# Performance work log

Hardware: AMD Instinct MI355X
Metric: run time of the kernel (lower is better)

## Reference

```python
import jax, jax.numpy as jnp
import numpy as np

HID = 1024
HEADS = 16
HEAD_DIM = HID // HEADS
LN_EPS = 1e-5  # nn.LayerNorm default (module's self.eps is unused by its LayerNorms)


def layer_norm(x, w, b):
    m = jnp.mean(x, axis=-1, keepdims=True)
    v = jnp.mean(jnp.square(x - m), axis=-1, keepdims=True)
    return (x - m) * jax.lax.rsqrt(v + LN_EPS) * w + b


def setup_inputs() -> dict:
    key = jax.random.key(0)
    ks = jax.random.split(key, 12)
    B, Nq, Nk = 2, 1024, 4096
    s = 1.0 / np.sqrt(HID)
    inp = {
        "queries": jax.random.normal(ks[0], (B, Nq, HID), jnp.float32),
        "kv_tokens": jax.random.normal(ks[1], (B, Nk, HID), jnp.float32),
        "query_type_ids": jax.random.randint(ks[2], (Nq,), 0, 3),
        "kv_type_ids": jax.random.randint(ks[3], (Nk,), 0, 3),
        "kv_padding_mask": jax.random.randint(ks[4], (B, Nk), 0, 2).astype(bool).at[:, 0].set(True),
        "Wq": jax.random.normal(ks[5], (HID, HID), jnp.float32) * s,
        "Wk": jax.random.normal(ks[6], (HID, HID), jnp.float32) * s,
        "Wv": jax.random.normal(ks[7], (HID, HID), jnp.float32) * s,
        "Wo": jax.random.normal(ks[8], (HID, HID), jnp.float32) * s,
        "qn_w": jnp.ones((HID,), jnp.float32), "qn_b": jnp.zeros((HID,), jnp.float32),
        "kvn_w": jnp.ones((HID,), jnp.float32), "kvn_b": jnp.zeros((HID,), jnp.float32),
        "on_w": jnp.ones((HID,), jnp.float32), "on_b": jnp.zeros((HID,), jnp.float32),
        "typed_bias": jax.random.normal(ks[9], (3, 3), jnp.float32) * 0.1,
    }
    return inp


def reference(queries, kv_tokens, query_type_ids, kv_type_ids, kv_padding_mask,
              Wq, Wk, Wv, Wo, qn_w, qn_b, kvn_w, kvn_b, on_w, on_b, typed_bias):
    B, Nq, D = queries.shape
    Nk = kv_tokens.shape[1]
    qn = layer_norm(queries, qn_w, qn_b)
    kvn = layer_norm(kv_tokens, kvn_w, kvn_b)
    # projections (torch Linear: x @ W.T), split heads -> [B, N, H, hd]
    q = (qn @ Wq.T).reshape(B, Nq, HEADS, HEAD_DIM)
    k = (kvn @ Wk.T).reshape(B, Nk, HEADS, HEAD_DIM)
    v = (kvn @ Wv.T).reshape(B, Nk, HEADS, HEAD_DIM)
    scale = 1.0 / jnp.sqrt(jnp.asarray(HEAD_DIM, queries.dtype))
    scores = jnp.einsum("bqhd,bkhd->bhqk", q, k) * scale  # [B,H,Nq,Nk]
    # additive mask: typed bias gather [Nq,Nk] + padding neg-inf [B,Nk]
    tbias = typed_bias[query_type_ids][:, kv_type_ids]  # [Nq,Nk]
    neg_inf = jnp.finfo(queries.dtype).min
    pad = jnp.where(kv_padding_mask[:, None, None, :], jnp.asarray(0.0, queries.dtype), neg_inf)
    attn = jax.nn.softmax(scores + tbias[None, None] + pad, axis=-1)
    out = jnp.einsum("bhqk,bkhd->bqhd", attn, v).reshape(B, Nq, D)
    out = out @ Wo.T
    return layer_norm(queries + out, on_w, on_b)
```

## Files before the change

kernel.cpp:

```cpp
#include <hip/hip_runtime.h>
#include <hip/hip_bf16.h>

#define HID   1024
#define NQ    1024
#define NK    4096
#define BB    2
#define HEADS 16
#define HD    64
#define LN_EPS 1e-5f
#define NEG_BIG (-1e9f)
#define SOFT_C 16.0f
#define KSPLIT 4
#define NKS   (NK / KSPLIT)
#define LOG2E 1.4426950408889634f
#define QSCALE_L2E 0.18033688f

typedef __bf16 bf16_t;
typedef bf16_t bf16x8 __attribute__((ext_vector_type(8)));
typedef bf16_t bf16x4 __attribute__((ext_vector_type(4)));
typedef float  f32x4  __attribute__((ext_vector_type(4)));

__device__ inline f32x4 mfma16(bf16x8 a, bf16x8 b, f32x4 c) {
    return __builtin_amdgcn_mfma_f32_16x16x32_bf16(a, b, c, 0, 0, 0);
}

__device__ inline void async_copy16(const bf16_t* g, bf16_t* l) {
    __builtin_amdgcn_global_load_lds(
        (const __attribute__((address_space(1))) void*)g,
        (__attribute__((address_space(3))) void*)l, 16, 0, 0);
}

__device__ inline void load4f(const void* p, int idx, int fl, float* o) {
    if (fl) {
        bf16x4 v = *(const bf16x4*)((const bf16_t*)p + idx);
#pragma unroll
        for (int i = 0; i < 4; i++) o[i] = (float)v[i];
    } else {
        float4 a = *(const float4*)((const float*)p + idx);
        o[0] = a.x; o[1] = a.y; o[2] = a.z; o[3] = a.w;
    }
}

__global__ void detect_kernel(const void* __restrict__ qnw,
                              const void* __restrict__ pad,
                              int* __restrict__ flags) {
    __shared__ int bad;
    if (threadIdx.x == 0) bad = 0;
    __syncthreads();
    const unsigned int* pw = (const unsigned int*)pad;
    int any = 0;
    for (int i = threadIdx.x; i < 2048; i += 256)
        if (pw[i] > 1u) any = 1;
    if (any) atomicOr(&bad, 1);
    __syncthreads();
    if (threadIdx.x == 0) {
        flags[0] = (*(const unsigned int*)qnw == 0x3F803F80u) ? 1 : 0;
        flags[1] = bad;
    }
}

__device__ inline float2 block_sum2(float a, float b) {
#pragma unroll
    for (int off = 32; off > 0; off >>= 1) {
        a += __shfl_down(a, off, 64);
        b += __shfl_down(b, off, 64);
    }
    __shared__ float sm[8];
    int w = threadIdx.x >> 6;
    if ((threadIdx.x & 63) == 0) { sm[w] = a; sm[w + 4] = b; }
    __syncthreads();
    float sa = sm[0] + sm[1] + sm[2] + sm[3];
    float sb = sm[4] + sm[5] + sm[6] + sm[7];
    return make_float2(sa, sb);
}

__global__ __launch_bounds__(256) void norm_rows_kernel(const void* __restrict__ x,
                                                        const void* __restrict__ lnw,
                                                        const void* __restrict__ lnb,
                                                        bf16_t* __restrict__ out,
                                                        const int* __restrict__ flags) {
    int fl = flags[0];
    int row = blockIdx.x;
    int t = threadIdx.x;
    float xf[4];
    load4f(x, row * HID + t * 4, fl, xf);
    float s = 0.f, s2 = 0.f;
#pragma unroll
    for (int i = 0; i < 4; i++) { s += xf[i]; s2 += xf[i] * xf[i]; }
    float2 sums = block_sum2(s, s2);
    float mean = sums.x * (1.0f / HID);
    float var  = fmaxf(sums.y * (1.0f / HID) - mean * mean, 0.f);
    float inv  = rsqrtf(var + LN_EPS);
    float wv[4], bv[4];
    load4f(lnw, t * 4, fl, wv);
    load4f(lnb, t * 4, fl, bv);
    bf16x4 o;
#pragma unroll
    for (int i = 0; i < 4; i++)
        o[i] = (bf16_t)((xf[i] - mean) * inv * wv[i] + bv[i]);
    *(bf16x4*)(out + (size_t)row * HID + t * 4) = o;
}

__global__ __launch_bounds__(256) void wconv_kernel(const void* __restrict__ w0,
                                                    const void* __restrict__ w1,
                                                    const void* __restrict__ w2,
                                                    const void* __restrict__ w3,
                                                    bf16_t* __restrict__ out,
                                                    const int* __restrict__ flags) {
    int z = blockIdx.y;
    const void* in = (z == 0) ? w0 : (z == 1) ? w1 : (z == 2) ? w2 : w3;
    bf16_t* o = out + (size_t)z * HID * HID;
    int i = (blockIdx.x * 256 + threadIdx.x) * 8;
    if (flags[0]) {
        *(uint4*)(o + i) = *(const uint4*)((const bf16_t*)in + i);
    } else {
        float4 a = *(const float4*)((const float*)in + i);
        float4 b = *(const float4*)((const float*)in + i + 4);
        bf16x8 v;
        v[0] = (bf16_t)a.x; v[1] = (bf16_t)a.y; v[2] = (bf16_t)a.z; v[3] = (bf16_t)a.w;
        v[4] = (bf16_t)b.x; v[5] = (bf16_t)b.y; v[6] = (bf16_t)b.z; v[7] = (bf16_t)b.w;
        *(bf16x8*)(o + i) = v;
    }
}

__global__ __launch_bounds__(256) void final_ln_kernel(const void* __restrict__ q,
                                                       const float* __restrict__ o2a,
                                                       const float* __restrict__ o2b,
                                                       const void* __restrict__ w,
                                                       const void* __restrict__ bias,
                                                       void* __restrict__ y,
                                                       const int* __restrict__ flags) {
    int fl = flags[0];
    int row = blockIdx.x;
    int t = threadIdx.x;
    float qf[4];
    load4f(q, row * HID + t * 4, fl, qf);
    float4 oa = *(const float4*)(o2a + (size_t)row * HID + t * 4);
    float4 ob = *(const float4*)(o2b + (size_t)row * HID + t * 4);
    float xf[4] = { qf[0] + oa.x + ob.x, qf[1] + oa.y + ob.y,
                    qf[2] + oa.z + ob.z, qf[3] + oa.w + ob.w };
    float s = 0.f, s2 = 0.f;
#pragma unroll
    for (int i = 0; i < 4; i++) { s += xf[i]; s2 += xf[i] * xf[i]; }
    float2 sums = block_sum2(s, s2);
    float mean = sums.x * (1.0f / HID);
    float var  = fmaxf(sums.y * (1.0f / HID) - mean * mean, 0.f);
    float inv  = rsqrtf(var + LN_EPS);
    float wv[4], bv[4];
    load4f(w, t * 4, fl, wv);
    load4f(bias, t * 4, fl, bv);
    if (fl) {
        bf16x4 out;
#pragma unroll
        for (int i = 0; i < 4; i++)
            out[i] = (bf16_t)((xf[i] - mean) * inv * wv[i] + bv[i]);
        *(bf16x4*)((bf16_t*)y + (size_t)row * HID + t * 4) = out;
    } else {
        float4 out;
        out.x = (xf[0] - mean) * inv * wv[0] + bv[0];
        out.y = (xf[1] - mean) * inv * wv[1] + bv[1];
        out.z = (xf[2] - mean) * inv * wv[2] + bv[2];
        out.w = (xf[3] - mean) * inv * wv[3] + bv[3];
        *(float4*)((float*)y + (size_t)row * HID + t * 4) = out;
    }
}

__global__ __launch_bounds__(256) void maskc_kernel(const int* __restrict__ kt,
                                                    const void* __restrict__ pad,
                                                    const void* __restrict__ tb,
                                                    float* __restrict__ mc,
                                                    const int* __restrict__ flags) {
    int fl = flags[0], padbyte = flags[1];
    int i = blockIdx.x * 256 + threadIdx.x;
    int tq  = i / (BB * NK);
    int rem = i - tq * (BB * NK);
    int b   = rem >> 12;
    int key = rem & (NK - 1);
    int ti = tq * 3 + kt[key];
    float v = fl ? (float)((const bf16_t*)tb)[ti] : ((const float*)tb)[ti];
    v = (v - SOFT_C) * LOG2E;
    bool ok = padbyte ? (((const unsigned char*)pad)[b * NK + key] != 0)
                      : (((const int*)pad)[b * NK + key] != 0);
    if (!ok) v = NEG_BIG;
    mc[i] = v;
}

__global__ __launch_bounds__(256) void gemm_qkv(const bf16_t* __restrict__ Aq,
                                                const bf16_t* __restrict__ Akv,
                                                const bf16_t* __restrict__ Wq,
                                                const bf16_t* __restrict__ Wkv,
                                                bf16_t* __restrict__ qp,
                                                bf16_t* __restrict__ kp,
                                                bf16_t* __restrict__ vT) {
    const int K = HID;
    __shared__ bf16_t As[128 * 32];
    __shared__ bf16_t Bs[128 * 32];
    int bid = blockIdx.x;
    bool isQ = bid < 128;
    const bf16_t* A; const bf16_t* W; int row0, col0;
    if (isQ) { A = Aq;  W = Wq;  row0 = (bid >> 3) * 128;  col0 = (bid & 7) * 128; }
    else     { int b2 = bid - 128;
               A = Akv; W = Wkv; row0 = (b2 >> 4) * 128;   col0 = (b2 & 15) * 128; }
    int t = threadIdx.x;
    int wave = t >> 6, lane = t & 63, quad = lane >> 4, l15 = lane & 15;
    int wr = wave >> 1, wc = wave & 1;

    int j0 = wave * 2;
    int srow = (lane >> 2);
    int skc  = (lane & 3) * 8;
    const bf16_t* Ag0 = A + (size_t)(row0 + 16 * j0 + srow) * K + skc;
    const bf16_t* Ag1 = Ag0 + (size_t)16 * K;
    const bf16_t* Bg0 = W + (size_t)(col0 + 16 * j0 + srow) * K + skc;
    const bf16_t* Bg1 = Bg0 + (size_t)16 * K;
    bf16_t* Asl0 = &As[j0 * 512];
    bf16_t* Asl1 = &As[j0 * 512 + 512];
    bf16_t* Bsl0 = &Bs[j0 * 512];
    bf16_t* Bsl1 = &Bs[j0 * 512 + 512];

    int aoff = (wr * 64 + l15) * 32 + quad * 8;
    int boff = (wc * 64 + l15) * 32 + quad * 8;

    f32x4 zero = {0.f, 0.f, 0.f, 0.f};
    f32x4 acc[4][4];
#pragma unroll
    for (int mt = 0; mt < 4; mt++)
#pragma unroll
        for (int nt = 0; nt < 4; nt++) acc[mt][nt] = zero;

    for (int k0 = 0; k0 < K; k0 += 32) {
        async_copy16(Ag0 + k0, Asl0);
        async_copy16(Ag1 + k0, Asl1);
        async_copy16(Bg0 + k0, Bsl0);
        async_copy16(Bg1 + k0, Bsl1);
        __syncthreads();
        bf16x8 a[4], b[4];
#pragma unroll
        for (int mt = 0; mt < 4; mt++) a[mt] = *(const bf16x8*)(&As[aoff + mt * 512]);
#pragma unroll
        for (int nt = 0; nt < 4; nt++) b[nt] = *(const bf16x8*)(&Bs[boff + nt * 512]);
#pragma unroll
        for (int mt = 0; mt < 4; mt++)
#pragma unroll
            for (int nt = 0; nt < 4; nt++)
                acc[mt][nt] = mfma16(a[mt], b[nt], acc[mt][nt]);
        __syncthreads();
    }

#pragma unroll
    for (int mt = 0; mt < 4; mt++) {
#pragma unroll
        for (int nt = 0; nt < 4; nt++) {
            int gr = row0 + wr * 64 + mt * 16 + quad * 4;
            int gc = col0 + wc * 64 + nt * 16 + l15;
            if (isQ) {
#pragma unroll
                for (int r = 0; r < 4; r++)
                    qp[(size_t)(gr + r) * HID + gc] = (bf16_t)acc[mt][nt][r];
            } else if (gc < 1024) {
#pragma unroll
                for (int r = 0; r < 4; r++)
                    kp[(size_t)(gr + r) * HID + gc] = (bf16_t)acc[mt][nt][r];
            } else {
                int dim = gc - 1024;
                int b = gr >> 12;
                int key = gr & (NK - 1);
                bf16x4 pk;
#pragma unroll
                for (int r = 0; r < 4; r++) pk[r] = (bf16_t)acc[mt][nt][r];
                *(bf16x4*)(vT + ((size_t)(b * HID + dim)) * NK + key) = pk;
            }
        }
    }
}

__global__ __launch_bounds__(256) void gemm_o(const bf16_t* __restrict__ A,
                                              const bf16_t* __restrict__ W,
                                              float* __restrict__ o2a,
                                              float* __restrict__ o2b) {
    const int K = HID;
    __shared__ bf16_t As[128 * 32];
    __shared__ bf16_t Bs[128 * 32];
    int row0 = blockIdx.x * 128, col0 = blockIdx.y * 128;
    int kbeg = blockIdx.z * (K / 2), kend = kbeg + K / 2;
    float* Co = blockIdx.z ? o2b : o2a;
    int t = threadIdx.x;
    int wave = t >> 6, lane = t & 63, quad = lane >> 4, l15 = lane & 15;
    int wr = wave >> 1, wc = wave & 1;

    int j0 = wave * 2;
    int srow = (lane >> 2);
    int skc  = (lane & 3) * 8;
    const bf16_t* Ag0 = A + (size_t)(row0 + 16 * j0 + srow) * K + skc;
    const bf16_t* Ag1 = Ag0 + (size_t)16 * K;
    const bf16_t* Bg0 = W + (size_t)(col0 + 16 * j0 + srow) * K + skc;
    const bf16_t* Bg1 = Bg0 + (size_t)16 * K;
    bf16_t* Asl0 = &As[j0 * 512];
    bf16_t* Asl1 = &As[j0 * 512 + 512];
    bf16_t* Bsl0 = &Bs[j0 * 512];
    bf16_t* Bsl1 = &Bs[j0 * 512 + 512];

    int aoff = (wr * 64 + l15) * 32 + quad * 8;
    int boff = (wc * 64 + l15) * 32 + quad * 8;

    f32x4 zero = {0.f, 0.f, 0.f, 0.f};
    f32x4 acc[4][4];
#pragma unroll
    for (int mt = 0; mt < 4; mt++)
#pragma unroll
        for (int nt = 0; nt < 4; nt++) acc[mt][nt] = zero;

    for (int k0 = kbeg; k0 < kend; k0 += 32) {
        async_copy16(Ag0 + k0, Asl0);
        async_copy16(Ag1 + k0, Asl1);
        async_copy16(Bg0 + k0, Bsl0);
        async_copy16(Bg1 + k0, Bsl1);
        __syncthreads();
        bf16x8 a[4], b[4];
#pragma unroll
        for (int mt = 0; mt < 4; mt++) a[mt] = *(const bf16x8*)(&As[aoff + mt * 512]);
#pragma unroll
        for (int nt = 0; nt < 4; nt++) b[nt] = *(const bf16x8*)(&Bs[boff + nt * 512]);
#pragma unroll
        for (int mt = 0; mt < 4; mt++)
#pragma unroll
            for (int nt = 0; nt < 4; nt++)
                acc[mt][nt] = mfma16(a[mt], b[nt], acc[mt][nt]);
        __syncthreads();
    }

#pragma unroll
    for (int mt = 0; mt < 4; mt++)
#pragma unroll
        for (int nt = 0; nt < 4; nt++) {
            int gr = row0 + wr * 64 + mt * 16 + quad * 4;
            int gc = col0 + wc * 64 + nt * 16 + l15;
#pragma unroll
            for (int r = 0; r < 4; r++)
                Co[(size_t)(gr + r) * HID + gc] = acc[mt][nt][r];
        }
}

__global__ __launch_bounds__(256) void attn_kernel(const bf16_t* __restrict__ q,
                                                   const bf16_t* __restrict__ kmat,
                                                   const bf16_t* __restrict__ vT,
                                                   const int* __restrict__ qt,
                                                   const float* __restrict__ mc,
                                                   bf16_t* __restrict__ Opart,
                                                   float* __restrict__ lpart) {
    int d   = blockIdx.x;
    int idx = ((d & 7) << 8) | (d >> 3);
    int q0  = (idx & 15) * 64;
    int h   = (idx >> 4) & 15;
    int zz  = idx >> 8;
    int b   = zz >> 2;
    int split = zz & (KSPLIT - 1);
    int t = threadIdx.x, wave = t >> 6, lane = t & 63, quad = lane >> 4, l15 = lane & 15;

    __shared__ bf16_t Ks[2][64 * 64];
    __shared__ bf16_t Vs[2][64 * 64];

    const bf16_t* qbase = q + ((size_t)(b * NQ + q0 + wave * 16 + l15)) * HID + h * HD + quad * 8;
    bf16x8 aq0 = *(const bf16x8*)(qbase);
    bf16x8 aq1 = *(const bf16x8*)(qbase + 32);

    int qi = q0 + wave * 16 + l15;
    const float* mrow = mc + ((size_t)qt[qi] * BB + b) * NK;

    f32x4 zero = {0.f, 0.f, 0.f, 0.f};
    f32x4 O[4] = {zero, zero, zero, zero};
    float l_ = 0.f;

    int kt_beg = split * NKS;
    const int NT = NKS / 64;

    int srow = wave * 16 + (lane >> 2);
    int sc2  = (lane & 3) * 2;
    int vsw = srow & 7;
    int vl0 = srow * 64 + ((sc2)     ^ vsw) * 8;
    int vl1 = srow * 64 + ((sc2 + 1) ^ vsw) * 8;
    int prow = (srow & 0x23) | ((srow & 4) << 2) | ((srow >> 1) & 0x0C);
    int ksw = prow & 7;
    int kl0 = prow * 64 + ((sc2)     ^ ksw) * 8;
    int kl1 = prow * 64 + ((sc2 + 1) ^ ksw) * 8;

    const bf16_t* kbase = kmat + ((size_t)(b * NK + kt_beg + srow)) * HID + h * HD + sc2 * 8;
    const bf16_t* vbase = vT + ((size_t)(b * HID + h * HD + srow)) * NK + kt_beg + sc2 * 8;
    const float*  mbase = mrow + kt_beg + (quad << 3);

    int fx = l15 & 7;
    int fA = l15 * 64 + ((quad) ^ fx) * 8;
    int fB = l15 * 64 + ((quad | 4) ^ fx) * 8;

    uint4 kA0, kA1, vA0, vA1;
    uint4 kB0, kB1, vB0, vB1;
    float4 mA[4], mB[4];

#define PKV(K0, K1, V0, V1, IT)                                              \
    if ((IT) < NT) {                                                         \
        const bf16_t* kp_ = kbase + (size_t)(IT) * 64 * HID;                 \
        const bf16_t* vp_ = vbase + (size_t)(IT) * 64;                       \
        K0 = *(const uint4*)(kp_); K1 = *(const uint4*)(kp_ + 8);            \
        V0 = *(const uint4*)(vp_); V1 = *(const uint4*)(vp_ + 8);            \
    }
#define PM(M, IT)                                                            \
    if ((IT) < NT) {                                                         \
        const float* mp_ = mbase + (size_t)(IT) * 64;                        \
        M[0] = *(const float4*)(mp_);                                        \
        M[1] = *(const float4*)(mp_ + 4);                                    \
        M[2] = *(const float4*)(mp_ + 32);                                   \
        M[3] = *(const float4*)(mp_ + 36);                                   \
    }
#define WKV(BUF, K0, K1, V0, V1, IT)                                         \
    if ((IT) < NT) {                                                         \
        *(uint4*)&Ks[BUF][kl0] = K0; *(uint4*)&Ks[BUF][kl1] = K1;            \
        *(uint4*)&Vs[BUF][vl0] = V0; *(uint4*)&Vs[BUF][vl1] = V1;            \
    }
#define BAR()                                                                \
    {                                                                        \
        asm volatile("s_waitcnt lgkmcnt(0)" ::: "memory");                   \
        __builtin_amdgcn_s_barrier();                                        \
    }
#define COMPUTE(BUF, M)                                                      \
    {                                                                        \
        const bf16_t* Kc = Ks[BUF];                                          \
        const bf16_t* Vc = Vs[BUF];                                          \
        f32x4 s4[4] = {zero, zero, zero, zero};                              \
        _Pragma("unroll")                                                    \
        for (int nt = 0; nt < 4; nt++) {                                     \
            bf16x8 k0 = *(const bf16x8*)(Kc + nt * 1024 + fA);               \
            bf16x8 k1 = *(const bf16x8*)(Kc + nt * 1024 + fB);               \
            s4[nt] = mfma16(k0, aq0, s4[nt]);                                \
            s4[nt] = mfma16(k1, aq1, s4[nt]);                                \
        }                                                                    \
        bf16x8 pa0, pa1;                                                     \
        _Pragma("unroll")                                                    \
        for (int nt = 0; nt < 4; nt++) {                                     \
            const float* mkp = (const float*)&M[nt];                         \
            _Pragma("unroll")                                                \
            for (int r = 0; r < 4; r++) {                                    \
                float p = exp2f(fmaf(s4[nt][r], QSCALE_L2E, mkp[r]));        \
                l_ += p;                                                     \
                bf16_t pb = (bf16_t)p;                                       \
                if (nt == 0)      pa0[r]     = pb;                           \
                else if (nt == 1) pa0[r + 4] = pb;                           \
                else if (nt == 2) pa1[r]     = pb;                           \
                else              pa1[r + 4] = pb;                           \
            }                                                                \
        }                                                                    \
        _Pragma("unroll")                                                    \
        for (int dt = 0; dt < 4; dt++) {                                     \
            bf16x8 v0 = *(const bf16x8*)(Vc + dt * 1024 + fA);               \
            bf16x8 v1 = *(const bf16x8*)(Vc + dt * 1024 + fB);               \
            O[dt] = mfma16(v0, pa0, O[dt]);                                  \
            O[dt] = mfma16(v1, pa1, O[dt]);                                  \
        }                                                                    \
    }

    PKV(kA0, kA1, vA0, vA1, 0);
    WKV(0, kA0, kA1, vA0, vA1, 0);
    PKV(kB0, kB1, vB0, vB1, 1);
    PM(mA, 0);

    for (int it = 0; it < NT; it += 2) {
        PM(mB, it + 1);
        PKV(kA0, kA1, vA0, vA1, it + 2);
        BAR();
        COMPUTE(0, mA);
        WKV(1, kB0, kB1, vB0, vB1, it + 1);
        PM(mA, it + 2);
        PKV(kB0, kB1, vB0, vB1, it + 3);
        BAR();
        COMPUTE(1, mB);
        WKV(0, kA0, kA1, vA0, vA1, it + 2);
    }

    size_t srow_base = (size_t)((split * BB + b) * HEADS + h) * NQ;
    float lf = l_;
    lf += __shfl_xor(lf, 16, 64);
    lf += __shfl_xor(lf, 32, 64);
    if (quad == 0) lpart[srow_base + qi] = lf;

    bf16_t* ob = &Ks[0][0] + wave * 1024;
#pragma unroll
    for (int dt = 0; dt < 4; dt++) {
        bf16x4 ov;
#pragma unroll
        for (int r = 0; r < 4; r++) ov[r] = (bf16_t)O[dt][r];
        *(bf16x4*)(ob + l15 * 64 + (((dt * 2 + (quad >> 1)) ^ fx) << 3) + ((quad & 1) << 2)) = ov;
    }
    int qq = lane >> 2, cc = lane & 3, sx = qq & 7;
    bf16x8 r0 = *(const bf16x8*)(ob + qq * 64 + (((cc * 2)     ^ sx) << 3));
    bf16x8 r1 = *(const bf16x8*)(ob + qq * 64 + (((cc * 2 + 1) ^ sx) << 3));
    size_t orow = (srow_base + (size_t)(q0 + wave * 16 + qq)) * HD + cc * 16;
    *(uint4*)(Opart + orow)     = *(uint4*)&r0;
    *(uint4*)(Opart + orow + 8) = *(uint4*)&r1;
#undef PKV
#undef PM
#undef WKV
#undef BAR
#undef COMPUTE
}

__global__ __launch_bounds__(256) void combine_kernel(const bf16_t* __restrict__ Opart,
                                                      const float* __restrict__ lpart,
                                                      bf16_t* __restrict__ ctx) {
    int wave = threadIdx.x >> 6, lane = threadIdx.x & 63;
    int rid = blockIdx.x * 4 + wave;
    int b   = rid >> 14;
    int rem = rid & 16383;
    int h   = rem >> 10;
    int qi  = rem & 1023;
    float o = 0.f, l = 0.f;
#pragma unroll
    for (int s = 0; s < KSPLIT; s++) {
        size_t idx = (size_t)((s * BB + b) * HEADS + h) * NQ + qi;
        l += lpart[idx];
        o += (float)Opart[idx * HD + lane];
    }
    ctx[(size_t)(b * NQ + qi) * HID + h * HD + lane] = (bf16_t)(o / l);
}

extern "C" void kernel_launch(void* const* d_in, const int* in_sizes, int n_in,
                              void* d_out, int out_size, void* d_ws, size_t ws_size,
                              hipStream_t stream) {
    (void)in_sizes; (void)n_in; (void)out_size; (void)ws_size;
    const void* queries = d_in[0];
    const void* kv      = d_in[1];
    const int* qt       = (const int*)d_in[2];
    const int* kt       = (const int*)d_in[3];
    const void* pad     = d_in[4];
    const void* Wq   = d_in[5];
    const void* Wk   = d_in[6];
    const void* Wv   = d_in[7];
    const void* Wo   = d_in[8];
    const void* qn_w = d_in[9];
    const void* qn_b = d_in[10];
    const void* kvn_w = d_in[11];
    const void* kvn_b = d_in[12];
    const void* on_w = d_in[13];
    const void* on_b = d_in[14];
    const void* tb   = d_in[15];

    char* ws = (char*)d_ws;
    bf16_t* q_c  = (bf16_t*)(ws);
    bf16_t* kv_c = (bf16_t*)(ws + ((size_t)4  << 20));
    bf16_t* ctx  = (bf16_t*)(ws + ((size_t)4  << 20));
    bf16_t* Wq_c = (bf16_t*)(ws + ((size_t)20 << 20));
    bf16_t* Wk_c = (bf16_t*)(ws + ((size_t)22 << 20));
    bf16_t* Wv_c = (bf16_t*)(ws + ((size_t)24 << 20));
    bf16_t* Wo_c = (bf16_t*)(ws + ((size_t)26 << 20));
    bf16_t* qp   = (bf16_t*)(ws + ((size_t)28 << 20));
    bf16_t* kp   = (bf16_t*)(ws + ((size_t)32 << 20));
    float*  o2a  = (float*)(ws + ((size_t)32 << 20));
    float*  o2b  = (float*)(ws + ((size_t)40 << 20));
    bf16_t* vT   = (bf16_t*)(ws + ((size_t)48 << 20));
    float*  mc   = (float*)(ws + ((size_t)64 << 20));
    int*    flags = (int*)(ws + ((size_t)64 << 20) + (256 << 10));
    bf16_t* Opart = (bf16_t*)(ws + ((size_t)65 << 20));
    float*  lbuf  = (float*)(ws + ((size_t)82 << 20));

    detect_kernel<<<1, 256, 0, stream>>>(qn_w, pad, flags);
    norm_rows_kernel<<<BB * NQ, 256, 0, stream>>>(queries, qn_w, qn_b, q_c, flags);
    norm_rows_kernel<<<BB * NK, 256, 0, stream>>>(kv, kvn_w, kvn_b, kv_c, flags);
    wconv_kernel<<<dim3(512, 4), 256, 0, stream>>>(Wq, Wk, Wv, Wo, Wq_c, flags);
    maskc_kernel<<<(3 * BB * NK) / 256, 256, 0, stream>>>(kt, pad, tb, mc, flags);
    gemm_qkv<<<1152, 256, 0, stream>>>(q_c, kv_c, Wq_c, Wk_c, qp, kp, vT);
    attn_kernel<<<dim3((NQ / 64) * HEADS * BB * KSPLIT), 256, 0, stream>>>(qp, kp, vT, qt, mc, Opart, lbuf);
    combine_kernel<<<(BB * HEADS * NQ) / 4, 256, 0, stream>>>(Opart, lbuf, ctx);
    gemm_o<<<dim3(16, 8, 2), 256, 0, stream>>>(ctx, Wo_c, o2a, o2b);
    final_ln_kernel<<<BB * NQ, 256, 0, stream>>>(queries, o2a, o2b, on_w, on_b, d_out, flags);
}
```

Before: 292.7 us.

## Split keys across waves with register-direct K/V loads and LDS reduction

The attention kernel now gives each wave all 64 queries and its own slice of keys. K and V fragments are loaded straight from global memory into registers with double buffering, so the shared-memory staging and per-tile barriers go away. Partial outputs and row sums from the four waves are reduced through a float LDS buffer at the end, and launch bounds ask for two blocks per CU. This trades barrier and LDS traffic for more register pressure, uncoalesced-ish per-lane global loads, and a larger LDS footprint for the final reduction.

```diff
diff --git a/kernel.cpp b/kernel.cpp
--- a/kernel.cpp
+++ b/kernel.cpp
@@ -340,13 +340,13 @@
         }
 }
 
-__global__ __launch_bounds__(256) void attn_kernel(const bf16_t* __restrict__ q,
-                                                   const bf16_t* __restrict__ kmat,
-                                                   const bf16_t* __restrict__ vT,
-                                                   const int* __restrict__ qt,
-                                                   const float* __restrict__ mc,
-                                                   bf16_t* __restrict__ Opart,
-                                                   float* __restrict__ lpart) {
+__global__ __launch_bounds__(256, 2) void attn_kernel(const bf16_t* __restrict__ q,
+                                                      const bf16_t* __restrict__ kmat,
+                                                      const bf16_t* __restrict__ vT,
+                                                      const int* __restrict__ qt,
+                                                      const float* __restrict__ mc,
+                                                      bf16_t* __restrict__ Opart,
+                                                      float* __restrict__ lpart) {
     int d   = blockIdx.x;
     int idx = ((d & 7) << 8) | (d >> 3);
     int q0  = (idx & 15) * 64;
@@ -354,151 +354,153 @@
     int zz  = idx >> 8;
     int b   = zz >> 2;
     int split = zz & (KSPLIT - 1);
-    int t = threadIdx.x, wave = t >> 6, lane = t & 63, quad = lane >> 4, l15 = lane & 15;
-
-    __shared__ bf16_t Ks[2][64 * 64];
-    __shared__ bf16_t Vs[2][64 * 64];
-
-    const bf16_t* qbase = q + ((size_t)(b * NQ + q0 + wave * 16 + l15)) * HID + h * HD + quad * 8;
-    bf16x8 aq0 = *(const bf16x8*)(qbase);
-    bf16x8 aq1 = *(const bf16x8*)(qbase + 32);
-
-    int qi = q0 + wave * 16 + l15;
-    const float* mrow = mc + ((size_t)qt[qi] * BB + b) * NK;
+    int lane = threadIdx.x & 63, w = threadIdx.x >> 6;
+    int quad = lane >> 4, l15 = lane & 15;
+
+    __shared__ float Osum[4][64][68];
+    __shared__ float lsum[4][4][16];
+
+    int kt_beg = split * NKS;
+    int key_w  = kt_beg + w * 32;
+
+    bf16x8 Qf[4][2];
+#pragma unroll
+    for (int qg = 0; qg < 4; qg++) {
+        const bf16_t* qb = q + ((size_t)(b * NQ + q0 + qg * 16 + l15)) * HID + h * HD + quad * 8;
+#pragma unroll
+        for (int kc = 0; kc < 2; kc++)
+            Qf[qg][kc] = *(const bf16x8*)(qb + kc * 32);
+    }
+
+    const float* mptr[4];
+#pragma unroll
+    for (int qg = 0; qg < 4; qg++) {
+        int qi = q0 + qg * 16 + l15;
+        mptr[qg] = mc + ((size_t)qt[qi] * BB + b) * NK + key_w + (quad << 3);
+    }
+
+    int kperm = ((l15 >> 2) << 3) | (l15 & 3);
+    const bf16_t* kptr[2][2];
+#pragma unroll
+    for (int kh = 0; kh < 2; kh++)
+#pragma unroll
+        for (int kc = 0; kc < 2; kc++)
+            kptr[kh][kc] = kmat + ((size_t)(b * NK + key_w + kperm + kh * 4)) * HID
+                           + h * HD + kc * 32 + quad * 8;
+
+    const bf16_t* vptr[4];
+#pragma unroll
+    for (int dg = 0; dg < 4; dg++)
+        vptr[dg] = vT + ((size_t)(b * HID + h * HD + dg * 16 + l15)) * NK + key_w + quad * 8;
 
     f32x4 zero = {0.f, 0.f, 0.f, 0.f};
-    f32x4 O[4] = {zero, zero, zero, zero};
-    float l_ = 0.f;
-
-    int kt_beg = split * NKS;
-    const int NT = NKS / 64;
-
-    int srow = wave * 16 + (lane >> 2);
-    int sc2  = (lane & 3) * 2;
-    int vsw = srow & 7;
-    int vl0 = srow * 64 + ((sc2)     ^ vsw) * 8;
-    int vl1 = srow * 64 + ((sc2 + 1) ^ vsw) * 8;
-    int prow = (srow & 0x23) | ((srow & 4) << 2) | ((srow >> 1) & 0x0C);
-    int ksw = prow & 7;
-    int kl0 = prow * 64 + ((sc2)     ^ ksw) * 8;
-    int kl1 = prow * 64 + ((sc2 + 1) ^ ksw) * 8;
-
-    const bf16_t* kbase = kmat + ((size_t)(b * NK + kt_beg + srow)) * HID + h * HD + sc2 * 8;
-    const bf16_t* vbase = vT + ((size_t)(b * HID + h * HD + srow)) * NK + kt_beg + sc2 * 8;
-    const float*  mbase = mrow + kt_beg + (quad << 3);
-
-    int fx = l15 & 7;
-    int fA = l15 * 64 + ((quad) ^ fx) * 8;
-    int fB = l15 * 64 + ((quad | 4) ^ fx) * 8;
-
-    uint4 kA0, kA1, vA0, vA1;
-    uint4 kB0, kB1, vB0, vB1;
-    float4 mA[4], mB[4];
-
-#define PKV(K0, K1, V0, V1, IT)                                              \
-    if ((IT) < NT) {                                                         \
-        const bf16_t* kp_ = kbase + (size_t)(IT) * 64 * HID;                 \
-        const bf16_t* vp_ = vbase + (size_t)(IT) * 64;                       \
-        K0 = *(const uint4*)(kp_); K1 = *(const uint4*)(kp_ + 8);            \
-        V0 = *(const uint4*)(vp_); V1 = *(const uint4*)(vp_ + 8);            \
-    }
-#define PM(M, IT)                                                            \
-    if ((IT) < NT) {                                                         \
-        const float* mp_ = mbase + (size_t)(IT) * 64;                        \
-        M[0] = *(const float4*)(mp_);                                        \
-        M[1] = *(const float4*)(mp_ + 4);                                    \
-        M[2] = *(const float4*)(mp_ + 32);                                   \
-        M[3] = *(const float4*)(mp_ + 36);                                   \
-    }
-#define WKV(BUF, K0, K1, V0, V1, IT)                                         \
-    if ((IT) < NT) {                                                         \
-        *(uint4*)&Ks[BUF][kl0] = K0; *(uint4*)&Ks[BUF][kl1] = K1;            \
-        *(uint4*)&Vs[BUF][vl0] = V0; *(uint4*)&Vs[BUF][vl1] = V1;            \
-    }
-#define BAR()                                                                \
+    f32x4 O[4][4];
+#pragma unroll
+    for (int dg = 0; dg < 4; dg++)
+#pragma unroll
+        for (int qg = 0; qg < 4; qg++) O[dg][qg] = zero;
+    float l_[4] = {0.f, 0.f, 0.f, 0.f};
+
+    bf16x8 kA[2][2], kB[2][2];
+
+#define LOADK(SET)                                                           \
+    _Pragma("unroll")                                                        \
+    for (int kh = 0; kh < 2; kh++)                                           \
+        _Pragma("unroll")                                                    \
+        for (int kc = 0; kc < 2; kc++) {                                     \
+            SET[kh][kc] = *(const bf16x8*)(kptr[kh][kc]);                    \
+            kptr[kh][kc] += 128 * HID;                                       \
+        }
+#define LOADVM(VF, MK)                                                       \
+    _Pragma("unroll")                                                        \
+    for (int dg = 0; dg < 4; dg++) {                                         \
+        VF[dg] = *(const bf16x8*)(vptr[dg]);                                 \
+        vptr[dg] += 128;                                                     \
+    }                                                                        \
+    _Pragma("unroll")                                                        \
+    for (int qg = 0; qg < 4; qg++) {                                         \
+        MK[qg][0] = *(const float4*)(mptr[qg]);                              \
+        MK[qg][1] = *(const float4*)(mptr[qg] + 4);                          \
+        mptr[qg] += 128;                                                     \
+    }
+#define COMPUTE(KF, VF, MK)                                                  \
     {                                                                        \
-        asm volatile("s_waitcnt lgkmcnt(0)" ::: "memory");                   \
-        __builtin_amdgcn_s_barrier();                                        \
-    }
-#define COMPUTE(BUF, M)                                                      \
-    {                                                                        \
-        const bf16_t* Kc = Ks[BUF];                                          \
-        const bf16_t* Vc = Vs[BUF];                                          \
-        f32x4 s4[4] = {zero, zero, zero, zero};                              \
+        bf16x8 P[4];                                                         \
         _Pragma("unroll")                                                    \
-        for (int nt = 0; nt < 4; nt++) {                                     \
-            bf16x8 k0 = *(const bf16x8*)(Kc + nt * 1024 + fA);               \
-            bf16x8 k1 = *(const bf16x8*)(Kc + nt * 1024 + fB);               \
-            s4[nt] = mfma16(k0, aq0, s4[nt]);                                \
-            s4[nt] = mfma16(k1, aq1, s4[nt]);                                \
-        }                                                                    \
-        bf16x8 pa0, pa1;                                                     \
-        _Pragma("unroll")                                                    \
-        for (int nt = 0; nt < 4; nt++) {                                     \
-            const float* mkp = (const float*)&M[nt];                         \
+        for (int qg = 0; qg < 4; qg++) {                                     \
             _Pragma("unroll")                                                \
-            for (int r = 0; r < 4; r++) {                                    \
-                float p = exp2f(fmaf(s4[nt][r], QSCALE_L2E, mkp[r]));        \
-                l_ += p;                                                     \
-                bf16_t pb = (bf16_t)p;                                       \
-                if (nt == 0)      pa0[r]     = pb;                           \
-                else if (nt == 1) pa0[r + 4] = pb;                           \
-                else if (nt == 2) pa1[r]     = pb;                           \
-                else              pa1[r + 4] = pb;                           \
+            for (int kh = 0; kh < 2; kh++) {                                 \
+                f32x4 s4 = mfma16(KF[kh][0], Qf[qg][0], zero);               \
+                s4 = mfma16(KF[kh][1], Qf[qg][1], s4);                       \
+                const float* mkp = (const float*)&MK[qg][kh];                \
+                _Pragma("unroll")                                            \
+                for (int r = 0; r < 4; r++) {                                \
+                    float p = exp2f(fmaf(s4[r], QSCALE_L2E, mkp[r]));        \
+                    l_[qg] += p;                                             \
+                    P[qg][kh * 4 + r] = (bf16_t)p;                           \
+                }                                                            \
             }                                                                \
         }                                                                    \
         _Pragma("unroll")                                                    \
-        for (int dt = 0; dt < 4; dt++) {                                     \
-            bf16x8 v0 = *(const bf16x8*)(Vc + dt * 1024 + fA);               \
-            bf16x8 v1 = *(const bf16x8*)(Vc + dt * 1024 + fB);               \
-            O[dt] = mfma16(v0, pa0, O[dt]);                                  \
-            O[dt] = mfma16(v1, pa1, O[dt]);                                  \
-        }                                                                    \
-    }
-
-    PKV(kA0, kA1, vA0, vA1, 0);
-    WKV(0, kA0, kA1, vA0, vA1, 0);
-    PKV(kB0, kB1, vB0, vB1, 1);
-    PM(mA, 0);
-
-    for (int it = 0; it < NT; it += 2) {
-        PM(mB, it + 1);
-        PKV(kA0, kA1, vA0, vA1, it + 2);
-        BAR();
-        COMPUTE(0, mA);
-        WKV(1, kB0, kB1, vB0, vB1, it + 1);
-        PM(mA, it + 2);
-        PKV(kB0, kB1, vB0, vB1, it + 3);
-        BAR();
-        COMPUTE(1, mB);
-        WKV(0, kA0, kA1, vA0, vA1, it + 2);
-    }
+        for (int dg = 0; dg < 4; dg++)                                       \
+            _Pragma("unroll")                                                \
+            for (int qg = 0; qg < 4; qg++)                                   \
+                O[dg][qg] = mfma16(VF[dg], P[qg], O[dg][qg]);                \
+    }
+
+    const int TILES = NKS / 128;
+    LOADK(kA);
+    for (int t = 0; t < TILES; t += 2) {
+        bf16x8 V0[4]; float4 m0[4][2];
+        LOADVM(V0, m0);
+        LOADK(kB);
+        COMPUTE(kA, V0, m0);
+        bf16x8 V1[4]; float4 m1[4][2];
+        LOADVM(V1, m1);
+        if (t + 2 < TILES) { LOADK(kA); }
+        COMPUTE(kB, V1, m1);
+    }
+#undef LOADK
+#undef LOADVM
+#undef COMPUTE
+
+#pragma unroll
+    for (int dg = 0; dg < 4; dg++)
+#pragma unroll
+        for (int qg = 0; qg < 4; qg++)
+            *(f32x4*)&Osum[w][qg * 16 + l15][dg * 16 + quad * 4] = O[dg][qg];
+#pragma unroll
+    for (int qg = 0; qg < 4; qg++) {
+        float lf = l_[qg];
+        lf += __shfl_xor(lf, 16, 64);
+        lf += __shfl_xor(lf, 32, 64);
+        if (quad == 0) lsum[w][qg][l15] = lf;
+    }
+    __syncthreads();
 
     size_t srow_base = (size_t)((split * BB + b) * HEADS + h) * NQ;
-    float lf = l_;
-    lf += __shfl_xor(lf, 16, 64);
-    lf += __shfl_xor(lf, 32, 64);
-    if (quad == 0) lpart[srow_base + qi] = lf;
-
-    bf16_t* ob = &Ks[0][0] + wave * 1024;
-#pragma unroll
-    for (int dt = 0; dt < 4; dt++) {
-        bf16x4 ov;
-#pragma unroll
-        for (int r = 0; r < 4; r++) ov[r] = (bf16_t)O[dt][r];
-        *(bf16x4*)(ob + l15 * 64 + (((dt * 2 + (quad >> 1)) ^ fx) << 3) + ((quad & 1) << 2)) = ov;
-    }
-    int qq = lane >> 2, cc = lane & 3, sx = qq & 7;
-    bf16x8 r0 = *(const bf16x8*)(ob + qq * 64 + (((cc * 2)     ^ sx) << 3));
-    bf16x8 r1 = *(const bf16x8*)(ob + qq * 64 + (((cc * 2 + 1) ^ sx) << 3));
-    size_t orow = (srow_base + (size_t)(q0 + wave * 16 + qq)) * HD + cc * 16;
-    *(uint4*)(Opart + orow)     = *(uint4*)&r0;
-    *(uint4*)(Opart + orow + 8) = *(uint4*)&r1;
-#undef PKV
-#undef PM
-#undef WKV
-#undef BAR
-#undef COMPUTE
+    int qq = lane >> 2, dq = lane & 3;
+    float acc[16];
+#pragma unroll
+    for (int i = 0; i < 16; i++) acc[i] = 0.f;
+#pragma unroll
+    for (int p = 0; p < 4; p++)
+#pragma unroll
+        for (int c = 0; c < 4; c++) {
+            f32x4 x = *(const f32x4*)&Osum[p][w * 16 + qq][dq * 16 + c * 4];
+#pragma unroll
+            for (int j = 0; j < 4; j++) acc[c * 4 + j] += x[j];
+        }
+    bf16x8 o0, o1;
+#pragma unroll
+    for (int j = 0; j < 8; j++) { o0[j] = (bf16_t)acc[j]; o1[j] = (bf16_t)acc[8 + j]; }
+    size_t orow = (srow_base + (size_t)(q0 + w * 16 + qq)) * HD + dq * 16;
+    *(uint4*)(Opart + orow)     = *(uint4*)&o0;
+    *(uint4*)(Opart + orow + 8) = *(uint4*)&o1;
+    if (dq == 0) {
+        float lt = lsum[0][w][qq] + lsum[1][w][qq] + lsum[2][w][qq] + lsum[3][w][qq];
+        lpart[srow_base + q0 + w * 16 + qq] = lt;
+    }
 }
 
 __global__ __launch_bounds__(256) void combine_kernel(const bf16_t* __restrict__ Opart,
```

After: 321.9 us. 1.1x slower.
